# Performance work log

Measured on AMD Instinct MI355X. Metric: run time of the kernel, lower is better.

## Reference

```python
import jax, jax.numpy as jnp
import numpy as np

ATTN_MULT = 8.0
NEG_INF = float('-inf')

N, Q, S, D = 16, 2048, 2048, 64


def setup_inputs() -> dict:
    key = jax.random.key(0)
    kq, kk, kv, kp = jax.random.split(key, 4)
    return {
        "queries_nqd": jax.random.normal(kq, (N, Q, D), dtype=jnp.float32),
        "keys_nsd": jax.random.normal(kk, (N, S, D), dtype=jnp.float32),
        "values_nsv": jax.random.normal(kv, (N, S, D), dtype=jnp.float32),
        "prefix_len_n": jax.random.randint(kp, (N,), 0, S, dtype=jnp.int64 if jax.config.jax_enable_x64 else jnp.int32),
    }


def reference(queries_nqd, keys_nsd, values_nsv, prefix_len_n):
    # attention_type == 'block_diagonal', backend == 'torch', dropout p == 0
    n, q, d = queries_nqd.shape
    s = keys_nsd.shape[1]
    scale = ATTN_MULT / d
    # prefix-block mask: key position < prefix_len (broadcast over queries)
    block_mask_n1s = (jnp.arange(s)[None, None, :] < prefix_len_n[:, None, None])  # [n,1,s]
    diag_mask_qs = jnp.arange(q)[:, None] == jnp.arange(s)[None, :]                # [q,s]
    mask_nqs = block_mask_n1s | diag_mask_qs[None, :, :]                           # [n,q,s]
    scores_nqs = jnp.einsum('nqd,nsd->nqs', queries_nqd, keys_nsd) * scale
    scores_nqs = jnp.where(mask_nqs, scores_nqs, NEG_INF)
    probs_nqs = jax.nn.softmax(scores_nqs, axis=-1)
    return jnp.einsum('nqs,nsv->nqv', probs_nqs, values_nsv)
```

## Files before the change

### kernel.cpp

```cpp
#include <hip/hip_runtime.h>
#include <hip/hip_bf16.h>
#include <math.h>

#define NH 16
#define QL 2048
#define SL 2048
#define DD 64
#define BQ 128
#define PSTR 72
#define QK_SCALE_LOG2E 0.1803368801111f

typedef __attribute__((ext_vector_type(8))) short short8;
typedef __attribute__((ext_vector_type(4))) float floatx4;
typedef __attribute__((ext_vector_type(4))) unsigned short ushort4v;
typedef __attribute__((ext_vector_type(8))) unsigned short ushort8v;

__device__ __forceinline__ unsigned short f2bf(float x) {
    unsigned u = __float_as_uint(x);
    u += 0x7FFFu + ((u >> 16) & 1u);
    return (unsigned short)(u >> 16);
}
__device__ __forceinline__ unsigned int f2bf2u(float x, float y) {
    __hip_bfloat162 h = __float22bfloat162_rn(make_float2(x, y));
    return *(unsigned int*)&h;
}
__device__ __forceinline__ float bf2f(unsigned short h) {
    return __uint_as_float((unsigned)h << 16);
}

__device__ __forceinline__ void gld16(const unsigned short* g, unsigned short* l) {
    __builtin_amdgcn_global_load_lds(
        (const __attribute__((address_space(1))) unsigned int*)g,
        (__attribute__((address_space(3))) unsigned int*)l, 16, 0, 0);
}

__global__ __launch_bounds__(256) void prep(
    const float* __restrict__ Kf, const float* __restrict__ Vf,
    unsigned short* __restrict__ Kb, unsigned short* __restrict__ Vtb)
{
    if (blockIdx.y == 0) {
        int idx = blockIdx.x * 256 + threadIdx.x;
        float4 v = ((const float4*)Kf)[idx];
        ushort4v h = { f2bf(v.x), f2bf(v.y), f2bf(v.z), f2bf(v.w) };
        *(ushort4v*)(Kb + (size_t)idx * 4) = h;
    } else {
        if (blockIdx.x >= 512) return;
        __shared__ unsigned short sT[64][PSTR];
        int bx = blockIdx.x;
        int n = bx >> 5, stile = bx & 31, s0 = stile * 64;
        int tid = (int)threadIdx.x;
        const float* vb = Vf + ((size_t)n * SL + s0) * DD;
        #pragma unroll
        for (int i = 0; i < 4; ++i) {
            int idx = tid + i * 256;
            int r = idx >> 4, c = (idx & 15) << 2;
            float4 v = *(const float4*)(vb + r * DD + c);
            sT[c + 0][r] = f2bf(v.x);
            sT[c + 1][r] = f2bf(v.y);
            sT[c + 2][r] = f2bf(v.z);
            sT[c + 3][r] = f2bf(v.w);
        }
        __syncthreads();
        int d = tid >> 2, sg = tid & 3;
        unsigned short* out = Vtb + (size_t)n * DD * SL + (size_t)d * SL + s0 + sg * 16;
        ushort8v a, b;
        #pragma unroll
        for (int i = 0; i < 8; ++i) { a[i] = sT[d][sg * 16 + i]; b[i] = sT[d][sg * 16 + 8 + i]; }
        *(ushort8v*)(out) = a;
        *(ushort8v*)(out + 8) = b;
    }
}

__global__ __launch_bounds__(512, 6) void attn_mfma_split(
    const float* __restrict__ Qf, const unsigned short* __restrict__ Kb,
    const unsigned short* __restrict__ Vtb, const int* __restrict__ plen_g,
    unsigned short* __restrict__ Opb, float* __restrict__ Lp, int spl)
{
    __shared__ unsigned short sK[2][64 * 64];
    __shared__ unsigned short sVt[2][64 * 64];
    __shared__ unsigned short sP[8 * 16 * 64];

    const int blk = blockIdx.x;
    const int n  = blk & (NH - 1);
    const int qt = blk >> 4;
    const int q0 = qt * BQ;
    const int sp = blockIdx.y;
    const int sbeg = sp * spl;
    const int plen = plen_g[n];
    const int ntile = spl >> 6;
    const bool hasdiag = (q0 >= sbeg) && (q0 < sbeg + spl);
    if (!((sbeg < plen) || hasdiag)) return;

    const int tid  = (int)threadIdx.x;
    const int wave = tid >> 6, lane = tid & 63, quad = lane >> 4, l16 = lane & 15;

    int rem  = plen - sbeg;
    int base = (rem > 0) ? min((rem + 63) >> 6, ntile) : 0;
    int td0 = -1, td1 = -1;
    if (hasdiag) {
        int d0 = (q0 - sbeg) >> 6;
        if (d0 >= base) td0 = d0;
        if (d0 + 1 >= base) td1 = d0 + 1;
    }
    const int total = base + (td0 >= 0) + (td1 >= 0);

    const int qrow  = wave * 16 + l16;
    const int qglob = q0 + qrow;
    const int pmask = (l16 & 7) * 8;

    short8 bQ0, bQ1;
    {
        const float* qf = Qf + ((size_t)(n * QL + qglob)) * DD + quad * 8;
        float4 a0 = *(const float4*)(qf);
        float4 a1 = *(const float4*)(qf + 4);
        float4 c0 = *(const float4*)(qf + 32);
        float4 c1 = *(const float4*)(qf + 36);
        const float S = QK_SCALE_LOG2E;
        unsigned int u0[4] = {
            f2bf2u(a0.x * S, a0.y * S), f2bf2u(a0.z * S, a0.w * S),
            f2bf2u(a1.x * S, a1.y * S), f2bf2u(a1.z * S, a1.w * S) };
        unsigned int u1[4] = {
            f2bf2u(c0.x * S, c0.y * S), f2bf2u(c0.z * S, c0.w * S),
            f2bf2u(c1.x * S, c1.y * S), f2bf2u(c1.z * S, c1.w * S) };
        bQ0 = *(short8*)u0;
        bQ1 = *(short8*)u1;
    }

    const unsigned short* kh = Kb  + (size_t)n * SL * DD;
    const unsigned short* vh = Vtb + (size_t)n * DD * SL;

    const int rr = wave * 8 + (lane >> 3);
    const int cg = ((lane & 7) ^ (rr & 7)) * 8;

    auto tile_of = [&](int i) -> int {
        if (i < base) return i;
        if (i == base) return (td0 >= 0) ? td0 : td1;
        return td1;
    };

    {
        int t0 = tile_of(0);
        const unsigned short* kg = kh + (size_t)(sbeg + t0 * 64) * DD;
        const unsigned short* vg = vh + (sbeg + t0 * 64);
        gld16(kg + rr * DD + cg, sK[0] + wave * 512);
        gld16(vg + (size_t)rr * SL + cg, sVt[0] + wave * 512);
    }

    floatx4 acc[4];
    #pragma unroll
    for (int dt = 0; dt < 4; ++dt) acc[dt] = (floatx4){0.f, 0.f, 0.f, 0.f};
    float lsum = 0.f;
    unsigned short* pw = sP + qrow * 64;

    for (int i = 0; i < total; ++i) {
        __syncthreads();

        if (i + 1 < total) {
            int tn = tile_of(i + 1);
            const unsigned short* kg = kh + (size_t)(sbeg + tn * 64) * DD;
            const unsigned short* vg = vh + (sbeg + tn * 64);
            gld16(kg + rr * DD + cg, sK[(i + 1) & 1] + wave * 512);
            gld16(vg + (size_t)rr * SL + cg, sVt[(i + 1) & 1] + wave * 512);
        }

        const unsigned short* sk = sK[i & 1];
        const unsigned short* sv = sVt[i & 1];
        const int t  = tile_of(i);
        const int s0 = sbeg + t * 64;

        floatx4 sf[4];
        #pragma unroll
        for (int st2 = 0; st2 < 4; ++st2) sf[st2] = (floatx4){0.f, 0.f, 0.f, 0.f};
        #pragma unroll
        for (int st2 = 0; st2 < 4; ++st2) {
            int krow = st2 * 16 + l16;
            short8 aK0 = *(const short8*)(sk + krow * 64 + (((0 * 4 + quad) ^ (krow & 7)) * 8));
            short8 aK1 = *(const short8*)(sk + krow * 64 + (((1 * 4 + quad) ^ (krow & 7)) * 8));
            sf[st2] = __builtin_amdgcn_mfma_f32_16x16x32_bf16(aK0, bQ0, sf[st2], 0, 0, 0);
            sf[st2] = __builtin_amdgcn_mfma_f32_16x16x32_bf16(aK1, bQ1, sf[st2], 0, 0, 0);
        }

        if (s0 + 64 <= plen) {
            #pragma unroll
            for (int st2 = 0; st2 < 4; ++st2) {
                float p0 = __builtin_amdgcn_exp2f(sf[st2][0]);
                float p1 = __builtin_amdgcn_exp2f(sf[st2][1]);
                float p2 = __builtin_amdgcn_exp2f(sf[st2][2]);
                float p3 = __builtin_amdgcn_exp2f(sf[st2][3]);
                lsum += (p0 + p1) + (p2 + p3);
                uint2 pk = { f2bf2u(p0, p1), f2bf2u(p2, p3) };
                *(uint2*)(pw + ((st2 * 16 + quad * 4) ^ pmask)) = pk;
            }
        } else {
            #pragma unroll
            for (int st2 = 0; st2 < 4; ++st2) {
                float p[4];
                #pragma unroll
                for (int r = 0; r < 4; ++r) {
                    int s = s0 + st2 * 16 + quad * 4 + r;
                    bool valid = (s < plen) || (s == qglob);
                    p[r] = __builtin_amdgcn_exp2f(valid ? sf[st2][r] : -INFINITY);
                    lsum += p[r];
                }
                uint2 pk = { f2bf2u(p[0], p[1]), f2bf2u(p[2], p[3]) };
                *(uint2*)(pw + ((st2 * 16 + quad * 4) ^ pmask)) = pk;
            }
        }

        #pragma unroll
        for (int ks = 0; ks < 2; ++ks) {
            short8 aP = *(const short8*)(pw + ((ks * 32 + quad * 8) ^ pmask));
            #pragma unroll
            for (int dt = 0; dt < 4; ++dt) {
                int vrow = dt * 16 + l16;
                short8 bV = *(const short8*)(sv + vrow * 64 + (((ks * 4 + quad) ^ (vrow & 7)) * 8));
                acc[dt] = __builtin_amdgcn_mfma_f32_16x16x32_bf16(aP, bV, acc[dt], 0, 0, 0);
            }
        }
    }

    lsum += __shfl_xor(lsum, 16, 64);
    lsum += __shfl_xor(lsum, 32, 64);
    if (quad == 0)
        Lp[((size_t)sp * NH + n) * QL + q0 + qrow] = lsum;

    unsigned short* pws = sP + wave * 16 * 64;
    #pragma unroll
    for (int dt = 0; dt < 4; ++dt) {
        int chunk = dt * 2 + (l16 >> 3);
        #pragma unroll
        for (int r = 0; r < 4; ++r) {
            int row = quad * 4 + r;
            int sw = ((chunk ^ (row & 7)) * 8) + (l16 & 7);
            pws[row * 64 + sw] = f2bf(acc[dt][r]);
        }
    }
    const size_t qbase = ((size_t)sp * NH + n) * QL + q0 + wave * 16;
    #pragma unroll
    for (int t = 0; t < 2; ++t) {
        int row = t * 8 + (lane >> 3);
        int chunk = lane & 7;
        int sw = (chunk ^ (row & 7)) * 8;
        ushort8v val = *(const ushort8v*)(pws + row * 64 + sw);
        *(ushort8v*)(Opb + (qbase + row) * DD + chunk * 8) = val;
    }
}

__global__ __launch_bounds__(256) void combine(
    const unsigned short* __restrict__ Opb, const float* __restrict__ Lp,
    const int* __restrict__ plen_g, float* __restrict__ Og, int nsplit, int spl)
{
    int idx = blockIdx.x * 256 + (int)threadIdx.x;
    int d4 = idx & 15;
    int q  = (idx >> 4) & (QL - 1);
    int n  = idx >> 15;
    int plen = plen_g[n];
    int spd = q / spl;
    float4 s = {0.f, 0.f, 0.f, 0.f};
    float l = 0.f;
    for (int sp = 0; sp < nsplit; ++sp) {
        if ((sp * spl < plen) || (sp == spd)) {
            const unsigned short* ob = Opb + (((size_t)sp * NH + n) * QL + q) * DD + d4 * 4;
            ushort4v v = *(const ushort4v*)(ob);
            s.x += bf2f(v[0]); s.y += bf2f(v[1]); s.z += bf2f(v[2]); s.w += bf2f(v[3]);
            l += Lp[((size_t)sp * NH + n) * QL + q];
        }
    }
    float inv = 1.0f / l;
    float4 o = { s.x * inv, s.y * inv, s.z * inv, s.w * inv };
    *(float4*)(Og + ((size_t)n * QL + q) * DD + d4 * 4) = o;
}

extern "C" void kernel_launch(void* const* d_in, const int* in_sizes, int n_in,
                              void* d_out, int out_size, void* d_ws, size_t ws_size,
                              hipStream_t stream) {
    const float* Qf   = (const float*)d_in[0];
    const float* Kf   = (const float*)d_in[1];
    const float* Vf   = (const float*)d_in[2];
    const int*   plen = (const int*)d_in[3];
    float* Og = (float*)d_out;

    char* ws = (char*)d_ws;
    unsigned short* Kb  = (unsigned short*)(ws);
    unsigned short* Vtb = (unsigned short*)(ws + (4u << 20));
    unsigned short* Opb = (unsigned short*)(ws + (8u << 20));

    const size_t op_bytes = (size_t)NH * QL * DD * 2;
    const size_t lp_bytes = (size_t)NH * QL * 4;
    int nsplit = 1;
    if (ws_size >= (8u << 20) + 4 * (op_bytes + lp_bytes)) nsplit = 4;
    else if (ws_size >= (8u << 20) + 2 * (op_bytes + lp_bytes)) nsplit = 2;
    float* Lp = (float*)(ws + (8u << 20) + (size_t)nsplit * op_bytes);
    int spl = SL / nsplit;

    prep<<<dim3(2048, 2), 256, 0, stream>>>(Kf, Vf, Kb, Vtb);
    attn_mfma_split<<<dim3(NH * (QL / BQ), nsplit), 512, 0, stream>>>(Qf, Kb, Vtb, plen, Opb, Lp, spl);
    combine<<<2048, 256, 0, stream>>>(Opb, Lp, plen, Og, nsplit, spl);
}
```

Measured before the change: 110.0 us.

## Fuse split-K combine into attention kernel via last-block atomic counter

Removes the separate combine kernel. The last split block for each query tile, found with an atomic counter plus threadfence, reduces the partial outputs and writes the final result. Tiles that have only one contributing split write normalized fp32 output directly, skipping the bf16 partial round trip. The prep grid is also compacted so no idle blocks are launched, and a memset resets the counters each call. This saves a kernel launch and partial-buffer traffic, at the cost of atomics and a serialized tail reduction in the last block.

```diff
diff --git a/kernel.cpp b/kernel.cpp
--- a/kernel.cpp
+++ b/kernel.cpp
@@ -38,15 +38,14 @@
     const float* __restrict__ Kf, const float* __restrict__ Vf,
     unsigned short* __restrict__ Kb, unsigned short* __restrict__ Vtb)
 {
-    if (blockIdx.y == 0) {
+    if (blockIdx.x < 2048) {
         int idx = blockIdx.x * 256 + threadIdx.x;
         float4 v = ((const float4*)Kf)[idx];
         ushort4v h = { f2bf(v.x), f2bf(v.y), f2bf(v.z), f2bf(v.w) };
         *(ushort4v*)(Kb + (size_t)idx * 4) = h;
     } else {
-        if (blockIdx.x >= 512) return;
         __shared__ unsigned short sT[64][PSTR];
-        int bx = blockIdx.x;
+        int bx = blockIdx.x - 2048;
         int n = bx >> 5, stile = bx & 31, s0 = stile * 64;
         int tid = (int)threadIdx.x;
         const float* vb = Vf + ((size_t)n * SL + s0) * DD;
@@ -74,11 +73,13 @@
 __global__ __launch_bounds__(512, 6) void attn_mfma_split(
     const float* __restrict__ Qf, const unsigned short* __restrict__ Kb,
     const unsigned short* __restrict__ Vtb, const int* __restrict__ plen_g,
-    unsigned short* __restrict__ Opb, float* __restrict__ Lp, int spl)
+    unsigned short* __restrict__ Opb, float* __restrict__ Lp, int* __restrict__ cnt,
+    float* __restrict__ Og, int nsplit, int spl)
 {
     __shared__ unsigned short sK[2][64 * 64];
     __shared__ unsigned short sVt[2][64 * 64];
     __shared__ unsigned short sP[8 * 16 * 64];
+    __shared__ int lastFlag;
 
     const int blk = blockIdx.x;
     const int n  = blk & (NH - 1);
@@ -88,11 +89,16 @@
     const int sbeg = sp * spl;
     const int plen = plen_g[n];
     const int ntile = spl >> 6;
-    const bool hasdiag = (q0 >= sbeg) && (q0 < sbeg + spl);
+    const int spd = q0 / spl;
+    const bool hasdiag = (sp == spd);
     if (!((sbeg < plen) || hasdiag)) return;
 
     const int tid  = (int)threadIdx.x;
     const int wave = tid >> 6, lane = tid & 63, quad = lane >> 4, l16 = lane & 15;
+
+    int contrib = 0;
+    for (int s = 0; s < nsplit; ++s)
+        contrib += ((s * spl < plen) || (s == spd)) ? 1 : 0;
 
     int rem  = plen - sbeg;
     int base = (rem > 0) ? min((rem + 63) >> 6, ntile) : 0;
@@ -221,6 +227,24 @@
 
     lsum += __shfl_xor(lsum, 16, 64);
     lsum += __shfl_xor(lsum, 32, 64);
+
+    if (contrib == 1) {
+        float lrow[4];
+        #pragma unroll
+        for (int r = 0; r < 4; ++r)
+            lrow[r] = __shfl(lsum, quad * 4 + r, 16);
+        float* ob = Og + ((size_t)n * QL + q0) * DD;
+        #pragma unroll
+        for (int r = 0; r < 4; ++r) {
+            float inv = 1.0f / lrow[r];
+            int ql = wave * 16 + quad * 4 + r;
+            #pragma unroll
+            for (int dt = 0; dt < 4; ++dt)
+                ob[(size_t)ql * DD + dt * 16 + l16] = acc[dt][r] * inv;
+        }
+        return;
+    }
+
     if (quad == 0)
         Lp[((size_t)sp * NH + n) * QL + q0 + qrow] = lsum;
 
@@ -244,31 +268,42 @@
         ushort8v val = *(const ushort8v*)(pws + row * 64 + sw);
         *(ushort8v*)(Opb + (qbase + row) * DD + chunk * 8) = val;
     }
-}
-
-__global__ __launch_bounds__(256) void combine(
-    const unsigned short* __restrict__ Opb, const float* __restrict__ Lp,
-    const int* __restrict__ plen_g, float* __restrict__ Og, int nsplit, int spl)
-{
-    int idx = blockIdx.x * 256 + (int)threadIdx.x;
-    int d4 = idx & 15;
-    int q  = (idx >> 4) & (QL - 1);
-    int n  = idx >> 15;
-    int plen = plen_g[n];
-    int spd = q / spl;
-    float4 s = {0.f, 0.f, 0.f, 0.f};
-    float l = 0.f;
-    for (int sp = 0; sp < nsplit; ++sp) {
-        if ((sp * spl < plen) || (sp == spd)) {
-            const unsigned short* ob = Opb + (((size_t)sp * NH + n) * QL + q) * DD + d4 * 4;
-            ushort4v v = *(const ushort4v*)(ob);
-            s.x += bf2f(v[0]); s.y += bf2f(v[1]); s.z += bf2f(v[2]); s.w += bf2f(v[3]);
-            l += Lp[((size_t)sp * NH + n) * QL + q];
-        }
-    }
-    float inv = 1.0f / l;
-    float4 o = { s.x * inv, s.y * inv, s.z * inv, s.w * inv };
-    *(float4*)(Og + ((size_t)n * QL + q) * DD + d4 * 4) = o;
+
+    __threadfence();
+    if (tid == 0) {
+        int old = atomicAdd(&cnt[blk], 1);
+        lastFlag = (old == contrib - 1);
+    }
+    __syncthreads();
+    if (!lastFlag) return;
+    __threadfence();
+
+    {
+        int row = tid >> 2;
+        int c0 = (tid & 3) * 16;
+        int q = q0 + row;
+        float l = 0.f;
+        float a2[16];
+        #pragma unroll
+        for (int j = 0; j < 16; ++j) a2[j] = 0.f;
+        for (int s = 0; s < nsplit; ++s) {
+            if ((s * spl < plen) || (s == spd)) {
+                const unsigned short* ob = Opb + (((size_t)s * NH + n) * QL + q) * DD + c0;
+                ushort8v v0 = *(const ushort8v*)(ob);
+                ushort8v v1 = *(const ushort8v*)(ob + 8);
+                #pragma unroll
+                for (int j = 0; j < 8; ++j) { a2[j] += bf2f(v0[j]); a2[8 + j] += bf2f(v1[j]); }
+                l += Lp[((size_t)s * NH + n) * QL + q];
+            }
+        }
+        float inv = 1.0f / l;
+        float* og = Og + ((size_t)n * QL + q) * DD + c0;
+        #pragma unroll
+        for (int j = 0; j < 4; ++j) {
+            float4 o = { a2[j * 4] * inv, a2[j * 4 + 1] * inv, a2[j * 4 + 2] * inv, a2[j * 4 + 3] * inv };
+            *(float4*)(og + j * 4) = o;
+        }
+    }
 }
 
 extern "C" void kernel_launch(void* const* d_in, const int* in_sizes, int n_in,
@@ -287,13 +322,16 @@
 
     const size_t op_bytes = (size_t)NH * QL * DD * 2;
     const size_t lp_bytes = (size_t)NH * QL * 4;
+    const size_t cnt_bytes = 256 * sizeof(int);
     int nsplit = 1;
-    if (ws_size >= (8u << 20) + 4 * (op_bytes + lp_bytes)) nsplit = 4;
-    else if (ws_size >= (8u << 20) + 2 * (op_bytes + lp_bytes)) nsplit = 2;
+    if (ws_size >= (8u << 20) + 4 * (op_bytes + lp_bytes) + cnt_bytes) nsplit = 4;
+    else if (ws_size >= (8u << 20) + 2 * (op_bytes + lp_bytes) + cnt_bytes) nsplit = 2;
     float* Lp = (float*)(ws + (8u << 20) + (size_t)nsplit * op_bytes);
+    int* cnt = (int*)(ws + (8u << 20) + (size_t)nsplit * (op_bytes + lp_bytes));
     int spl = SL / nsplit;
 
-    prep<<<dim3(2048, 2), 256, 0, stream>>>(Kf, Vf, Kb, Vtb);
-    attn_mfma_split<<<dim3(NH * (QL / BQ), nsplit), 512, 0, stream>>>(Qf, Kb, Vtb, plen, Opb, Lp, spl);
-    combine<<<2048, 256, 0, stream>>>(Opb, Lp, plen, Og, nsplit, spl);
-}
+    hipMemsetAsync(cnt, 0, cnt_bytes, stream);
+    prep<<<2560, 256, 0, stream>>>(Kf, Vf, Kb, Vtb);
+    attn_mfma_split<<<dim3(NH * (QL / BQ), nsplit), 512, 0, stream>>>(
+        Qf, Kb, Vtb, plen, Opb, Lp, cnt, Og, nsplit, spl);
+}
```

New measurement: 332.1 us. 202% more time.
